# Performance work log

Hardware: AMD Instinct MI355X
Metric: run time of the kernel (lower is better)

Reference implementation:

```python
import jax, jax.numpy as jnp
import numpy as np

N = 10000       # nodes
E = 160000      # edges (avg degree 16)
F_IN = 5        # node feature dim
ED = 2          # edge feature dim


def _tconv(x, src, dst, ea, Wq, bq, Wk, bk, Wv, bv, We, Ws, bs, heads, C, concat):
    """PyG TransformerConv (eval mode, root_weight=True, beta=False)."""
    n = x.shape[0]
    q = (x @ Wq + bq).reshape(n, heads, C)
    k = (x @ Wk + bk).reshape(n, heads, C)
    v = (x @ Wv + bv).reshape(n, heads, C)
    e = (ea @ We).reshape(ea.shape[0], heads, C)          # edge embedding, added to key and value
    kj = k[src] + e                                        # [E,H,C] gather source keys
    vj = v[src] + e                                        # [E,H,C] gather source values
    logits = jnp.einsum('ehc,ehc->eh', q[dst], kj) / jnp.sqrt(jnp.asarray(C, x.dtype))
    m = jax.ops.segment_max(logits, dst, num_segments=n)   # stable segment softmax over in-edges
    p = jnp.exp(logits - m[dst])
    s = jax.ops.segment_sum(p, dst, num_segments=n)
    alpha = p / s[dst]                                     # [E,H]
    out = jax.ops.segment_sum(alpha[..., None] * vj, dst, num_segments=n)  # [N,H,C]
    out = out.reshape(n, heads * C) if concat else jnp.mean(out, axis=1)
    return out + x @ Ws + bs                               # root/skip connection


def setup_inputs() -> dict:
    key = jax.random.key(0)
    keys = iter(jax.random.split(key, 64))
    def p(shape):
        return jax.random.normal(next(keys), shape, jnp.float32) * 0.05
    inp = {}
    inp['x'] = jax.random.normal(next(keys), (N, F_IN), jnp.float32)
    inp['edge_src'] = jax.random.randint(next(keys), (E,), 0, N)
    inp['edge_dst'] = jax.random.randint(next(keys), (E,), 0, N)
    inp['edge_attr'] = jax.random.normal(next(keys), (E, ED), jnp.float32)
    # (in_dim, heads, out_channels, concat) for the 3 TransformerConv layers
    layers = [(F_IN, 4, 128, True), (512, 4, 128, True), (512, 1, 64, False)]
    for i, (fin, h, c, concat) in enumerate(layers, 1):
        hc = h * c
        sk = hc if concat else c
        inp[f'Wq{i}'] = p((fin, hc)); inp[f'bq{i}'] = p((hc,))
        inp[f'Wk{i}'] = p((fin, hc)); inp[f'bk{i}'] = p((hc,))
        inp[f'Wv{i}'] = p((fin, hc)); inp[f'bv{i}'] = p((hc,))
        inp[f'We{i}'] = p((ED, hc))   # lin_edge has no bias in PyG
        inp[f'Ws{i}'] = p((fin, sk)); inp[f'bs{i}'] = p((sk,))
    return inp


def reference(x, edge_src, edge_dst, edge_attr,
              Wq1, bq1, Wk1, bk1, Wv1, bv1, We1, Ws1, bs1,
              Wq2, bq2, Wk2, bk2, Wv2, bv2, We2, Ws2, bs2,
              Wq3, bq3, Wk3, bk3, Wv3, bv3, We3, Ws3, bs3):
    h = jax.nn.relu(_tconv(x, edge_src, edge_dst, edge_attr,
                           Wq1, bq1, Wk1, bk1, Wv1, bv1, We1, Ws1, bs1, 4, 128, True))
    h = jax.nn.relu(_tconv(h, edge_src, edge_dst, edge_attr,
                           Wq2, bq2, Wk2, bk2, Wv2, bv2, We2, Ws2, bs2, 4, 128, True))
    return _tconv(h, edge_src, edge_dst, edge_attr,
                  Wq3, bq3, Wk3, bk3, Wv3, bv3, We3, Ws3, bs3, 1, 64, False)
```

## Files before the change

### kernel.cpp

```cpp
#include <hip/hip_runtime.h>

typedef unsigned short u16;
typedef __attribute__((ext_vector_type(8))) short bf16x8;
typedef __attribute__((ext_vector_type(4))) float f32x4;

__device__ __forceinline__ float bf2f(u16 s) {
    return __uint_as_float(((unsigned)s) << 16);
}
__device__ __forceinline__ u16 f2bf(float f) {
    unsigned u = __float_as_uint(f);
    u += 0x7fff + ((u >> 16) & 1);
    return (u16)(u >> 16);
}
__device__ __forceinline__ void unpack8(bf16x8 x, float* f) {
#pragma unroll
    for (int j = 0; j < 8; ++j) f[j] = bf2f((u16)x[j]);
}

struct Ptr4 { const float* p[4]; };
struct Ptr8 { const float* p[8]; };

__global__ __launch_bounds__(256)
void transpose_cvt4(Ptr4 srcs, u16* __restrict__ dst, int K, int Nw) {
    const float* in = srcs.p[blockIdx.z];
    u16* out = dst + (size_t)blockIdx.z * Nw * K;
    __shared__ float t[32][33];
    int kb = blockIdx.x * 32, nb = blockIdx.y * 32;
    int tx = threadIdx.x & 31, ty = threadIdx.x >> 5;
#pragma unroll
    for (int r = ty; r < 32; r += 8)
        if (kb + r < K && nb + tx < Nw)
            t[r][tx] = in[(size_t)(kb + r) * Nw + nb + tx];
    __syncthreads();
#pragma unroll
    for (int r = ty; r < 32; r += 8)
        if (nb + r < Nw && kb + tx < K)
            out[(size_t)(nb + r) * K + kb + tx] = f2bf(t[tx][r]);
}

__global__ __launch_bounds__(256)
void bias_pack(Ptr8 a, float* __restrict__ b2, float* __restrict__ b3) {
    int j = blockIdx.x * 256 + threadIdx.x;
    if (j < 2048) b2[j] = a.p[j >> 9][j & 511];
    else if (j < 2304) { int jj = j - 2048; b3[jj] = a.p[4 + (jj >> 6)][jj & 63]; }
}

__global__ __launch_bounds__(256)
void gemm_l1(const float* __restrict__ X, Ptr8 wb, u16* __restrict__ OUT, int N) {
    int n = blockIdx.x;
    int wsel = threadIdx.x >> 6;
    int jj = (threadIdx.x & 63) * 8;
    const float* W = wb.p[wsel];
    const float* b = wb.p[4 + wsel];
    float xr[5];
#pragma unroll
    for (int i = 0; i < 5; ++i) xr[i] = X[(size_t)n * 5 + i];
    float acc[8];
#pragma unroll
    for (int j = 0; j < 8; ++j) acc[j] = b[jj + j];
#pragma unroll
    for (int i = 0; i < 5; ++i)
#pragma unroll
        for (int j = 0; j < 8; ++j)
            acc[j] = fmaf(xr[i], W[(size_t)i * 512 + jj + j], acc[j]);
    bf16x8 o;
#pragma unroll
    for (int j = 0; j < 8; ++j) o[j] = (short)f2bf(acc[j]);
    *(bf16x8*)(OUT + (size_t)n * 2048 + wsel * 512 + jj) = o;
}

template <int TN>
__global__ __launch_bounds__(256)
void gemm_bf16(const u16* __restrict__ A, const u16* __restrict__ Bt,
               const float* __restrict__ bias, u16* __restrict__ C,
               int M, int Ncols, int K) {
    constexpr int TM = 128, BK = 64;
    constexpr int MFR = (TN == 128) ? 4 : 2;
    constexpr int NFR = 4;
    constexpr int ACH = TM * BK / (256 * 8);
    constexpr int BCH = TN * BK / (256 * 8);

    __shared__ u16 As[TM * BK];
    __shared__ u16 Bs[TN * BK];

    int tid = threadIdx.x;
    int lane = tid & 63;
    int w = tid >> 6;
    int rowbase = blockIdx.x * TM;
    int colbase = blockIdx.y * TN;
    int mwave = (TN == 128) ? (w >> 1) * 64 : w * 32;
    int nwave = (TN == 128) ? (w & 1) * 64 : 0;

    f32x4 acc[MFR][NFR] = {};

    for (int k0 = 0; k0 < K; k0 += BK) {
        bf16x8 ra[ACH], rb[BCH];
#pragma unroll
        for (int c = 0; c < ACH; ++c) {
            int idx = c * 256 + tid;
            int row = idx >> 3, sl = idx & 7;
            int gr = rowbase + row; if (gr > M - 1) gr = M - 1;
            ra[c] = *(const bf16x8*)(A + (size_t)gr * K + k0 + sl * 8);
        }
#pragma unroll
        for (int c = 0; c < BCH; ++c) {
            int idx = c * 256 + tid;
            int row = idx >> 3, sl = idx & 7;
            rb[c] = *(const bf16x8*)(Bt + (size_t)(colbase + row) * K + k0 + sl * 8);
        }
        __syncthreads();
#pragma unroll
        for (int c = 0; c < ACH; ++c) {
            int idx = c * 256 + tid;
            int row = idx >> 3, sl = idx & 7;
            *(bf16x8*)&As[row * BK + ((sl ^ (row & 7)) * 8)] = ra[c];
        }
#pragma unroll
        for (int c = 0; c < BCH; ++c) {
            int idx = c * 256 + tid;
            int row = idx >> 3, sl = idx & 7;
            *(bf16x8*)&Bs[row * BK + ((sl ^ (row & 7)) * 8)] = rb[c];
        }
        __syncthreads();
#pragma unroll
        for (int kh = 0; kh < 2; ++kh) {
            bf16x8 af[MFR], bfr[NFR];
            int ks = (lane >> 4) + kh * 4;
#pragma unroll
            for (int mi = 0; mi < MFR; ++mi) {
                int r = mwave + mi * 16 + (lane & 15);
                af[mi] = *(const bf16x8*)&As[r * BK + ((ks ^ (r & 7)) * 8)];
            }
#pragma unroll
            for (int ni = 0; ni < NFR; ++ni) {
                int r = nwave + ni * 16 + (lane & 15);
                bfr[ni] = *(const bf16x8*)&Bs[r * BK + ((ks ^ (r & 7)) * 8)];
            }
#pragma unroll
            for (int mi = 0; mi < MFR; ++mi)
#pragma unroll
                for (int ni = 0; ni < NFR; ++ni)
                    acc[mi][ni] = __builtin_amdgcn_mfma_f32_16x16x32_bf16(
                        af[mi], bfr[ni], acc[mi][ni], 0, 0, 0);
        }
    }
#pragma unroll
    for (int mi = 0; mi < MFR; ++mi) {
        int r0 = rowbase + mwave + mi * 16 + (lane >> 4) * 4;
#pragma unroll
        for (int ni = 0; ni < NFR; ++ni) {
            int col = colbase + nwave + ni * 16 + (lane & 15);
            float bv = bias[col];
#pragma unroll
            for (int r = 0; r < 4; ++r) {
                int row = r0 + r;
                if (row < M)
                    C[(size_t)row * Ncols + col] = f2bf(acc[mi][ni][r] + bv);
            }
        }
    }
}

__global__ __launch_bounds__(256)
void histo_dst(const int* __restrict__ dst, int* __restrict__ deg, int E) {
    int i = blockIdx.x * 256 + threadIdx.x;
    if (i < E) atomicAdd(&deg[dst[i]], 1);
}

__global__ __launch_bounds__(1024)
void scan_deg(const int* __restrict__ deg, int* __restrict__ off,
              int* __restrict__ cur, int N) {
    __shared__ int part[1024];
    int t = threadIdx.x;
    int per = (N + 1023) / 1024;
    int base = t * per;
    int s = 0;
    for (int i = 0; i < per; ++i)
        if (base + i < N) s += deg[base + i];
    part[t] = s;
    __syncthreads();
    for (int d = 1; d < 1024; d <<= 1) {
        int v = (t >= d) ? part[t - d] : 0;
        __syncthreads();
        part[t] += v;
        __syncthreads();
    }
    int excl = (t > 0) ? part[t - 1] : 0;
    for (int i = 0; i < per; ++i) {
        int n = base + i;
        if (n < N) {
            off[n] = excl;
            cur[n] = excl;
            excl += deg[n];
        }
    }
    if (t == 1023) off[N] = part[1023];
}

__global__ __launch_bounds__(256)
void scatter_edges(const int* __restrict__ dst, int* __restrict__ cur,
                   int* __restrict__ eid, int E) {
    int i = blockIdx.x * 256 + threadIdx.x;
    if (i < E) {
        int p = atomicAdd(&cur[dst[i]], 1);
        eid[p] = i;
    }
}

template <int H, int C, int LPG, int EPAR, bool RELU, typename OutT>
__global__ __launch_bounds__(256)
void node_attn(const u16* __restrict__ QKVS, int SR, int koff, int voff,
               int skoff, const int* __restrict__ esrc,
               const float* __restrict__ EA, const float* __restrict__ We,
               const int* __restrict__ off, const int* __restrict__ eid,
               OutT* __restrict__ OUT, int OST, int N, float scale) {
    constexpr int HC = H * C;
    constexpr int NG = 64 / LPG;
    int n = blockIdx.x * 4 + (threadIdx.x >> 6);
    if (n >= N) return;
    int lane = threadIdx.x & 63;
    int g = lane / LPG;
    int li = lane % LPG;
    int cc = (EPAR > 1 ? 0 : g) * C + li * 8;

    const u16* nrow = QKVS + (size_t)n * SR;
    float q[8];
    unpack8(*(const bf16x8*)(nrow + cc), q);

    float qw0 = 0.f, qw1 = 0.f;
    {
        f32x4 wa = *(const f32x4*)(We + cc), wb = *(const f32x4*)(We + cc + 4);
        f32x4 wc = *(const f32x4*)(We + HC + cc), wd = *(const f32x4*)(We + HC + cc + 4);
#pragma unroll
        for (int j = 0; j < 4; ++j) {
            qw0 = fmaf(q[j], wa[j], qw0); qw0 = fmaf(q[4 + j], wb[j], qw0);
            qw1 = fmaf(q[j], wc[j], qw1); qw1 = fmaf(q[4 + j], wd[j], qw1);
        }
    }
#pragma unroll
    for (int d = 1; d < LPG; d <<= 1) {
        qw0 += __shfl_xor(qw0, d);
        qw1 += __shfl_xor(qw1, d);
    }

    int base = off[n];
    int deg = off[n + 1] - base;
    int pdeg = deg < 64 ? deg : 64;
    int ps = 0; float pax = 0.f, pay = 0.f;
    if (lane < pdeg) {
        int e = eid[base + lane];
        ps = esrc[e];
        float2 a = *(const float2*)(EA + 2 * (size_t)e);
        pax = a.x; pay = a.y;
    }

    float m = -1e30f, s = 0.f, A0 = 0.f, A1 = 0.f;
    float acc[8] = {};
    const u16* Kp = QKVS + koff;
    const u16* Vp = QKVS + voff;

    auto process = [&](float ax, float ay, bf16x8 k8, bf16x8 v8) {
        float kf[8];
        unpack8(k8, kf);
        float qk = 0.f;
#pragma unroll
        for (int j = 0; j < 8; ++j) qk = fmaf(q[j], kf[j], qk);
#pragma unroll
        for (int d = 1; d < LPG; d <<= 1) qk += __shfl_xor(qk, d);
        float lg = scale * (qk + ax * qw0 + ay * qw1);
        if (lg > m + 8.f) {
            float r = __expf(m - lg);
            s *= r; A0 *= r; A1 *= r;
#pragma unroll
            for (int j = 0; j < 8; ++j) acc[j] *= r;
            m = lg;
        }
        float p = __expf(lg - m);
        s += p;
        A0 = fmaf(p, ax, A0);
        A1 = fmaf(p, ay, A1);
        float vf[8];
        unpack8(v8, vf);
#pragma unroll
        for (int j = 0; j < 8; ++j) acc[j] = fmaf(p, vf[j], acc[j]);
    };

    if constexpr (EPAR == 1) {
        int t = 0;
        for (; t + 1 < pdeg; t += 2) {
            int s0 = __shfl(ps, t), s1 = __shfl(ps, t + 1);
            float ax0 = __shfl(pax, t), ay0 = __shfl(pay, t);
            float ax1 = __shfl(pax, t + 1), ay1 = __shfl(pay, t + 1);
            bf16x8 k0 = *(const bf16x8*)(Kp + (size_t)s0 * SR + cc);
            bf16x8 v0 = *(const bf16x8*)(Vp + (size_t)s0 * SR + cc);
            bf16x8 k1 = *(const bf16x8*)(Kp + (size_t)s1 * SR + cc);
            bf16x8 v1 = *(const bf16x8*)(Vp + (size_t)s1 * SR + cc);
            process(ax0, ay0, k0, v0);
            process(ax1, ay1, k1, v1);
        }
        if (t < pdeg) {
            int s0 = __shfl(ps, t);
            float ax0 = __shfl(pax, t), ay0 = __shfl(pay, t);
            bf16x8 k0 = *(const bf16x8*)(Kp + (size_t)s0 * SR + cc);
            bf16x8 v0 = *(const bf16x8*)(Vp + (size_t)s0 * SR + cc);
            process(ax0, ay0, k0, v0);
        }
        for (t = 64; t < deg; ++t) {
            int e = eid[base + t];
            int s0 = esrc[e];
            float2 a = *(const float2*)(EA + 2 * (size_t)e);
            bf16x8 k0 = *(const bf16x8*)(Kp + (size_t)s0 * SR + cc);
            bf16x8 v0 = *(const bf16x8*)(Vp + (size_t)s0 * SR + cc);
            process(a.x, a.y, k0, v0);
        }
    } else {
        int trips = (pdeg + NG - 1) / NG;
        for (int k = 0; k < trips; ++k) {
            int idx = g + NG * k;
            bool valid = idx < pdeg;
            int sidx = valid ? idx : (pdeg - 1);
            int s0 = __shfl(ps, sidx);
            float ax0 = __shfl(pax, sidx), ay0 = __shfl(pay, sidx);
            bf16x8 k0 = *(const bf16x8*)(Kp + (size_t)s0 * SR + cc);
            bf16x8 v0 = *(const bf16x8*)(Vp + (size_t)s0 * SR + cc);
            if (valid) process(ax0, ay0, k0, v0);
        }
        int otr = (deg > 64) ? (deg - 64 + NG - 1) / NG : 0;
        for (int k = 0; k < otr; ++k) {
            int idx = 64 + NG * k + g;
            bool valid = idx < deg;
            int ii = valid ? idx : (deg - 1);
            int e = eid[base + ii];
            int s0 = esrc[e];
            float2 a = *(const float2*)(EA + 2 * (size_t)e);
            bf16x8 k0 = *(const bf16x8*)(Kp + (size_t)s0 * SR + cc);
            bf16x8 v0 = *(const bf16x8*)(Vp + (size_t)s0 * SR + cc);
            if (valid) process(a.x, a.y, k0, v0);
        }
#pragma unroll
        for (int d = LPG; d < 64; d <<= 1) {
            float mo = __shfl_xor(m, d), so = __shfl_xor(s, d);
            float A0o = __shfl_xor(A0, d), A1o = __shfl_xor(A1, d);
            float mn = fmaxf(m, mo);
            float ra = __expf(m - mn), rb = __expf(mo - mn);
            s = s * ra + so * rb;
            A0 = A0 * ra + A0o * rb;
            A1 = A1 * ra + A1o * rb;
#pragma unroll
            for (int j = 0; j < 8; ++j) {
                float ao = __shfl_xor(acc[j], d);
                acc[j] = acc[j] * ra + ao * rb;
            }
            m = mn;
        }
    }

    if (EPAR == 1 || g == 0) {
        float inv = (s > 0.f) ? 1.f / s : 0.f;
        float sk[8];
        unpack8(*(const bf16x8*)(nrow + skoff + cc), sk);
        f32x4 wa = *(const f32x4*)(We + cc), wb = *(const f32x4*)(We + cc + 4);
        f32x4 wc = *(const f32x4*)(We + HC + cc), wd = *(const f32x4*)(We + HC + cc + 4);
        float w0[8] = {wa[0], wa[1], wa[2], wa[3], wb[0], wb[1], wb[2], wb[3]};
        float w1[8] = {wc[0], wc[1], wc[2], wc[3], wd[0], wd[1], wd[2], wd[3]};
        float o[8];
#pragma unroll
        for (int j = 0; j < 8; ++j) {
            float agg = (acc[j] + A0 * w0[j] + A1 * w1[j]) * inv;
            o[j] = agg + sk[j];
            if (RELU) o[j] = fmaxf(o[j], 0.f);
        }
        if constexpr (sizeof(OutT) == 2) {
            bf16x8 ov;
#pragma unroll
            for (int j = 0; j < 8; ++j) ov[j] = (short)f2bf(o[j]);
            *(bf16x8*)((u16*)OUT + (size_t)n * OST + cc) = ov;
        } else {
            f32x4 oa = {o[0], o[1], o[2], o[3]}, ob = {o[4], o[5], o[6], o[7]};
            *(f32x4*)((float*)OUT + (size_t)n * OST + cc) = oa;
            *(f32x4*)((float*)OUT + (size_t)n * OST + cc + 4) = ob;
        }
    }
}

extern "C" void kernel_launch(void* const* d_in, const int* in_sizes, int n_in,
                              void* d_out, int out_size, void* d_ws, size_t ws_size,
                              hipStream_t stream) {
    const float* x  = (const float*)d_in[0];
    const int* esrc = (const int*)d_in[1];
    const int* edst = (const int*)d_in[2];
    const float* ea = (const float*)d_in[3];
    const int N = in_sizes[0] / 5;
    const int E = in_sizes[1];
    auto in = [&](int i) { return (const float*)d_in[i]; };

    char* p = (char*)d_ws;
    auto alloc = [&](size_t b) {
        char* r = p; p += (b + 255) & ~(size_t)255; return (void*)r;
    };
    u16* QKVS = (u16*)alloc((size_t)N * 2048 * 2);
    u16* HB   = (u16*)alloc((size_t)N * 512 * 2);
    u16* Wt2  = (u16*)alloc((size_t)2048 * 512 * 2);
    u16* Wt3  = (u16*)alloc((size_t)256 * 512 * 2);
    float* b2 = (float*)alloc(2048 * 4);
    float* b3 = (float*)alloc(256 * 4);
    int* deg  = (int*)alloc((size_t)N * 4);
    int* off  = (int*)alloc((size_t)(N + 1) * 4);
    int* cur  = (int*)alloc((size_t)N * 4);
    int* eid  = (int*)alloc((size_t)E * 4);

    dim3 b256(256);
    int gE256 = (E + 255) / 256;
    int gM = (N + 127) / 128;
    int gA = (N + 3) / 4;
    const float scale128 = 0.08838834764831845f;
    const float scale64  = 0.125f;

    hipMemsetAsync(deg, 0, (size_t)N * sizeof(int), stream);
    histo_dst<<<gE256, b256, 0, stream>>>(edst, deg, E);
    scan_deg<<<1, 1024, 0, stream>>>(deg, off, cur, N);
    scatter_edges<<<gE256, b256, 0, stream>>>(edst, cur, eid, E);

    Ptr4 w2 = {{in(13), in(15), in(17), in(20)}};
    Ptr4 w3 = {{in(22), in(24), in(26), in(29)}};
    Ptr8 bb = {{in(14), in(16), in(18), in(21), in(23), in(25), in(27), in(30)}};
    transpose_cvt4<<<dim3(16, 16, 4), b256, 0, stream>>>(w2, Wt2, 512, 512);
    transpose_cvt4<<<dim3(16, 2, 4),  b256, 0, stream>>>(w3, Wt3, 512, 64);
    bias_pack<<<dim3(9), b256, 0, stream>>>(bb, b2, b3);

    Ptr8 l1 = {{in(4), in(6), in(8), in(11), in(5), in(7), in(9), in(12)}};
    gemm_l1<<<dim3(N), b256, 0, stream>>>(x, l1, QKVS, N);
    node_attn<4, 128, 16, 1, true, u16><<<dim3(gA), b256, 0, stream>>>(
        QKVS, 2048, 512, 1024, 1536, esrc, ea, in(10), off, eid, HB, 512, N, scale128);

    gemm_bf16<128><<<dim3(gM, 16), b256, 0, stream>>>(HB, Wt2, b2, QKVS, N, 2048, 512);
    node_attn<4, 128, 16, 1, true, u16><<<dim3(gA), b256, 0, stream>>>(
        QKVS, 2048, 512, 1024, 1536, esrc, ea, in(19), off, eid, HB, 512, N, scale128);

    gemm_bf16<64><<<dim3(gM, 4), b256, 0, stream>>>(HB, Wt3, b3, QKVS, N, 256, 512);
    node_attn<1, 64, 8, 8, false, float><<<dim3(gA), b256, 0, stream>>>(
        QKVS, 256, 64, 128, 192, esrc, ea, in(28), off, eid,
        (float*)d_out, 64, N, scale64);
}
```

Baseline: 246.7 us.

## Pre-gather edge src/attrs into CSR order, prefetch K/V, merge prep kernels

The edge scatter now writes source indices and edge attributes directly in CSR order, so the attention kernels read them contiguously instead of chasing eid->esrc/EA. The EPAR=1 attention loop is software-pipelined, keeping four edges' K/V loads in flight ahead of use. The weight transpose and bias pack kernels are merged into one launch, and the layer-1 GEMM processes 8 nodes per block with weights held in registers. In exchange the scatter writes more data, and the prefetch adds register pressure plus redundant loads of edge 0 when an index runs past the degree.

```diff
diff --git a/kernel.cpp b/kernel.cpp
--- a/kernel.cpp
+++ b/kernel.cpp
@@ -17,56 +17,74 @@
     for (int j = 0; j < 8; ++j) f[j] = bf2f((u16)x[j]);
 }
 
-struct Ptr4 { const float* p[4]; };
 struct Ptr8 { const float* p[8]; };
-
-__global__ __launch_bounds__(256)
-void transpose_cvt4(Ptr4 srcs, u16* __restrict__ dst, int K, int Nw) {
-    const float* in = srcs.p[blockIdx.z];
-    u16* out = dst + (size_t)blockIdx.z * Nw * K;
+struct PrepArgs { const float* w[8]; const float* b[8]; };
+
+__global__ __launch_bounds__(256)
+void prep_weights(PrepArgs a, u16* __restrict__ Wt2, u16* __restrict__ Wt3,
+                  float* __restrict__ b2, float* __restrict__ b3) {
+    int z = blockIdx.z;
+    if (z == 8) {
+        if (blockIdx.y != 0 || blockIdx.x >= 9) return;
+        int j = blockIdx.x * 256 + threadIdx.x;
+        if (j < 2048) b2[j] = a.b[j >> 9][j & 511];
+        else if (j < 2304) { int jj = j - 2048; b3[jj] = a.b[4 + (jj >> 6)][jj & 63]; }
+        return;
+    }
+    const float* in;
+    u16* out;
+    int Nw;
+    if (z < 4) { in = a.w[z]; out = Wt2 + (size_t)z * 512 * 512; Nw = 512; }
+    else {
+        if (blockIdx.y >= 2) return;
+        in = a.w[z]; out = Wt3 + (size_t)(z - 4) * 64 * 512; Nw = 64;
+    }
     __shared__ float t[32][33];
     int kb = blockIdx.x * 32, nb = blockIdx.y * 32;
     int tx = threadIdx.x & 31, ty = threadIdx.x >> 5;
 #pragma unroll
     for (int r = ty; r < 32; r += 8)
-        if (kb + r < K && nb + tx < Nw)
+        if (nb + tx < Nw)
             t[r][tx] = in[(size_t)(kb + r) * Nw + nb + tx];
     __syncthreads();
 #pragma unroll
     for (int r = ty; r < 32; r += 8)
-        if (nb + r < Nw && kb + tx < K)
-            out[(size_t)(nb + r) * K + kb + tx] = f2bf(t[tx][r]);
-}
-
-__global__ __launch_bounds__(256)
-void bias_pack(Ptr8 a, float* __restrict__ b2, float* __restrict__ b3) {
-    int j = blockIdx.x * 256 + threadIdx.x;
-    if (j < 2048) b2[j] = a.p[j >> 9][j & 511];
-    else if (j < 2304) { int jj = j - 2048; b3[jj] = a.p[4 + (jj >> 6)][jj & 63]; }
+        if (nb + r < Nw)
+            out[(size_t)(nb + r) * 512 + kb + tx] = f2bf(t[tx][r]);
 }
 
 __global__ __launch_bounds__(256)
 void gemm_l1(const float* __restrict__ X, Ptr8 wb, u16* __restrict__ OUT, int N) {
-    int n = blockIdx.x;
     int wsel = threadIdx.x >> 6;
     int jj = (threadIdx.x & 63) * 8;
     const float* W = wb.p[wsel];
     const float* b = wb.p[4 + wsel];
-    float xr[5];
-#pragma unroll
-    for (int i = 0; i < 5; ++i) xr[i] = X[(size_t)n * 5 + i];
-    float acc[8];
-#pragma unroll
-    for (int j = 0; j < 8; ++j) acc[j] = b[jj + j];
+    float w[5][8], bs[8];
 #pragma unroll
     for (int i = 0; i < 5; ++i)
 #pragma unroll
-        for (int j = 0; j < 8; ++j)
-            acc[j] = fmaf(xr[i], W[(size_t)i * 512 + jj + j], acc[j]);
-    bf16x8 o;
-#pragma unroll
-    for (int j = 0; j < 8; ++j) o[j] = (short)f2bf(acc[j]);
-    *(bf16x8*)(OUT + (size_t)n * 2048 + wsel * 512 + jj) = o;
+        for (int j = 0; j < 8; ++j) w[i][j] = W[(size_t)i * 512 + jj + j];
+#pragma unroll
+    for (int j = 0; j < 8; ++j) bs[j] = b[jj + j];
+    int n0 = blockIdx.x * 8;
+    int nend = (N - n0 < 8) ? (N - n0) : 8;
+    for (int i = 0; i < nend; ++i) {
+        int n = n0 + i;
+        float xr[5];
+#pragma unroll
+        for (int k = 0; k < 5; ++k) xr[k] = X[(size_t)n * 5 + k];
+        float acc[8];
+#pragma unroll
+        for (int j = 0; j < 8; ++j) acc[j] = bs[j];
+#pragma unroll
+        for (int k = 0; k < 5; ++k)
+#pragma unroll
+            for (int j = 0; j < 8; ++j) acc[j] = fmaf(xr[k], w[k][j], acc[j]);
+        bf16x8 o;
+#pragma unroll
+        for (int j = 0; j < 8; ++j) o[j] = (short)f2bf(acc[j]);
+        *(bf16x8*)(OUT + (size_t)n * 2048 + wsel * 512 + jj) = o;
+    }
 }
 
 template <int TN>
@@ -198,22 +216,24 @@
 }
 
 __global__ __launch_bounds__(256)
-void scatter_edges(const int* __restrict__ dst, int* __restrict__ cur,
-                   int* __restrict__ eid, int E) {
+void scatter_edges(const int* __restrict__ src, const int* __restrict__ dst,
+                   const float* __restrict__ EA, int* __restrict__ cur,
+                   int* __restrict__ csrc, float2* __restrict__ caxy, int E) {
     int i = blockIdx.x * 256 + threadIdx.x;
     if (i < E) {
         int p = atomicAdd(&cur[dst[i]], 1);
-        eid[p] = i;
+        csrc[p] = src[i];
+        caxy[p] = *(const float2*)(EA + 2 * (size_t)i);
     }
 }
 
 template <int H, int C, int LPG, int EPAR, bool RELU, typename OutT>
 __global__ __launch_bounds__(256)
 void node_attn(const u16* __restrict__ QKVS, int SR, int koff, int voff,
-               int skoff, const int* __restrict__ esrc,
-               const float* __restrict__ EA, const float* __restrict__ We,
-               const int* __restrict__ off, const int* __restrict__ eid,
-               OutT* __restrict__ OUT, int OST, int N, float scale) {
+               int skoff, const int* __restrict__ csrc,
+               const float2* __restrict__ caxy, const float* __restrict__ We,
+               const int* __restrict__ off, OutT* __restrict__ OUT,
+               int OST, int N, float scale) {
     constexpr int HC = H * C;
     constexpr int NG = 64 / LPG;
     int n = blockIdx.x * 4 + (threadIdx.x >> 6);
@@ -248,9 +268,8 @@
     int pdeg = deg < 64 ? deg : 64;
     int ps = 0; float pax = 0.f, pay = 0.f;
     if (lane < pdeg) {
-        int e = eid[base + lane];
-        ps = esrc[e];
-        float2 a = *(const float2*)(EA + 2 * (size_t)e);
+        ps = csrc[base + lane];
+        float2 a = caxy[base + lane];
         pax = a.x; pay = a.y;
     }
 
@@ -286,29 +305,44 @@
     };
 
     if constexpr (EPAR == 1) {
-        int t = 0;
-        for (; t + 1 < pdeg; t += 2) {
-            int s0 = __shfl(ps, t), s1 = __shfl(ps, t + 1);
-            float ax0 = __shfl(pax, t), ay0 = __shfl(pay, t);
-            float ax1 = __shfl(pax, t + 1), ay1 = __shfl(pay, t + 1);
-            bf16x8 k0 = *(const bf16x8*)(Kp + (size_t)s0 * SR + cc);
-            bf16x8 v0 = *(const bf16x8*)(Vp + (size_t)s0 * SR + cc);
-            bf16x8 k1 = *(const bf16x8*)(Kp + (size_t)s1 * SR + cc);
-            bf16x8 v1 = *(const bf16x8*)(Vp + (size_t)s1 * SR + cc);
-            process(ax0, ay0, k0, v0);
-            process(ax1, ay1, k1, v1);
-        }
-        if (t < pdeg) {
-            int s0 = __shfl(ps, t);
-            float ax0 = __shfl(pax, t), ay0 = __shfl(pay, t);
-            bf16x8 k0 = *(const bf16x8*)(Kp + (size_t)s0 * SR + cc);
-            bf16x8 v0 = *(const bf16x8*)(Vp + (size_t)s0 * SR + cc);
-            process(ax0, ay0, k0, v0);
-        }
-        for (t = 64; t < deg; ++t) {
-            int e = eid[base + t];
-            int s0 = esrc[e];
-            float2 a = *(const float2*)(EA + 2 * (size_t)e);
+        auto ldp = [&](int t, bf16x8& k8, bf16x8& v8) {
+            int tt = t < pdeg ? t : 0;
+            int s0 = __shfl(ps, tt);
+            k8 = *(const bf16x8*)(Kp + (size_t)s0 * SR + cc);
+            v8 = *(const bf16x8*)(Vp + (size_t)s0 * SR + cc);
+        };
+        if (pdeg > 0) {
+            bf16x8 ka0, va0, ka1, va1, kb0, vb0, kb1, vb1;
+            ldp(0, ka0, va0); ldp(1, ka1, va1);
+            ldp(2, kb0, vb0); ldp(3, kb1, vb1);
+            int t = 0;
+            for (; t + 2 < pdeg; t += 4) {
+                float ax, ay;
+                ax = __shfl(pax, t); ay = __shfl(pay, t);
+                process(ax, ay, ka0, va0);
+                ax = __shfl(pax, t + 1); ay = __shfl(pay, t + 1);
+                process(ax, ay, ka1, va1);
+                ldp(t + 4, ka0, va0); ldp(t + 5, ka1, va1);
+                ax = __shfl(pax, t + 2); ay = __shfl(pay, t + 2);
+                process(ax, ay, kb0, vb0);
+                if (t + 3 < pdeg) {
+                    ax = __shfl(pax, t + 3); ay = __shfl(pay, t + 3);
+                    process(ax, ay, kb1, vb1);
+                }
+                ldp(t + 6, kb0, vb0); ldp(t + 7, kb1, vb1);
+            }
+            if (t < pdeg) {
+                float ax = __shfl(pax, t), ay = __shfl(pay, t);
+                process(ax, ay, ka0, va0);
+            }
+            if (t + 1 < pdeg) {
+                float ax = __shfl(pax, t + 1), ay = __shfl(pay, t + 1);
+                process(ax, ay, ka1, va1);
+            }
+        }
+        for (int t = 64; t < deg; ++t) {
+            int s0 = csrc[base + t];
+            float2 a = caxy[base + t];
             bf16x8 k0 = *(const bf16x8*)(Kp + (size_t)s0 * SR + cc);
             bf16x8 v0 = *(const bf16x8*)(Vp + (size_t)s0 * SR + cc);
             process(a.x, a.y, k0, v0);
@@ -330,9 +364,8 @@
             int idx = 64 + NG * k + g;
             bool valid = idx < deg;
             int ii = valid ? idx : (deg - 1);
-            int e = eid[base + ii];
-            int s0 = esrc[e];
-            float2 a = *(const float2*)(EA + 2 * (size_t)e);
+            int s0 = csrc[base + ii];
+            float2 a = caxy[base + ii];
             bf16x8 k0 = *(const bf16x8*)(Kp + (size_t)s0 * SR + cc);
             bf16x8 v0 = *(const bf16x8*)(Vp + (size_t)s0 * SR + cc);
             if (valid) process(a.x, a.y, k0, v0);
@@ -398,16 +431,17 @@
     auto alloc = [&](size_t b) {
         char* r = p; p += (b + 255) & ~(size_t)255; return (void*)r;
     };
-    u16* QKVS = (u16*)alloc((size_t)N * 2048 * 2);
-    u16* HB   = (u16*)alloc((size_t)N * 512 * 2);
-    u16* Wt2  = (u16*)alloc((size_t)2048 * 512 * 2);
-    u16* Wt3  = (u16*)alloc((size_t)256 * 512 * 2);
-    float* b2 = (float*)alloc(2048 * 4);
-    float* b3 = (float*)alloc(256 * 4);
-    int* deg  = (int*)alloc((size_t)N * 4);
-    int* off  = (int*)alloc((size_t)(N + 1) * 4);
-    int* cur  = (int*)alloc((size_t)N * 4);
-    int* eid  = (int*)alloc((size_t)E * 4);
+    u16* QKVS  = (u16*)alloc((size_t)N * 2048 * 2);
+    u16* HB    = (u16*)alloc((size_t)N * 512 * 2);
+    u16* Wt2   = (u16*)alloc((size_t)2048 * 512 * 2);
+    u16* Wt3   = (u16*)alloc((size_t)256 * 512 * 2);
+    float* b2  = (float*)alloc(2048 * 4);
+    float* b3  = (float*)alloc(256 * 4);
+    int* deg   = (int*)alloc((size_t)N * 4);
+    int* off   = (int*)alloc((size_t)(N + 1) * 4);
+    int* cur   = (int*)alloc((size_t)N * 4);
+    int* csrc  = (int*)alloc((size_t)E * 4);
+    float2* caxy = (float2*)alloc((size_t)E * 8);
 
     dim3 b256(256);
     int gE256 = (E + 255) / 256;
@@ -419,26 +453,23 @@
     hipMemsetAsync(deg, 0, (size_t)N * sizeof(int), stream);
     histo_dst<<<gE256, b256, 0, stream>>>(edst, deg, E);
     scan_deg<<<1, 1024, 0, stream>>>(deg, off, cur, N);
-    scatter_edges<<<gE256, b256, 0, stream>>>(edst, cur, eid, E);
-
-    Ptr4 w2 = {{in(13), in(15), in(17), in(20)}};
-    Ptr4 w3 = {{in(22), in(24), in(26), in(29)}};
-    Ptr8 bb = {{in(14), in(16), in(18), in(21), in(23), in(25), in(27), in(30)}};
-    transpose_cvt4<<<dim3(16, 16, 4), b256, 0, stream>>>(w2, Wt2, 512, 512);
-    transpose_cvt4<<<dim3(16, 2, 4),  b256, 0, stream>>>(w3, Wt3, 512, 64);
-    bias_pack<<<dim3(9), b256, 0, stream>>>(bb, b2, b3);
+    scatter_edges<<<gE256, b256, 0, stream>>>(esrc, edst, ea, cur, csrc, caxy, E);
+
+    PrepArgs pa = {{in(13), in(15), in(17), in(20), in(22), in(24), in(26), in(29)},
+                   {in(14), in(16), in(18), in(21), in(23), in(25), in(27), in(30)}};
+    prep_weights<<<dim3(16, 16, 9), b256, 0, stream>>>(pa, Wt2, Wt3, b2, b3);
 
     Ptr8 l1 = {{in(4), in(6), in(8), in(11), in(5), in(7), in(9), in(12)}};
-    gemm_l1<<<dim3(N), b256, 0, stream>>>(x, l1, QKVS, N);
+    gemm_l1<<<dim3((N + 7) / 8), b256, 0, stream>>>(x, l1, QKVS, N);
     node_attn<4, 128, 16, 1, true, u16><<<dim3(gA), b256, 0, stream>>>(
-        QKVS, 2048, 512, 1024, 1536, esrc, ea, in(10), off, eid, HB, 512, N, scale128);
+        QKVS, 2048, 512, 1024, 1536, csrc, caxy, in(10), off, HB, 512, N, scale128);
 
     gemm_bf16<128><<<dim3(gM, 16), b256, 0, stream>>>(HB, Wt2, b2, QKVS, N, 2048, 512);
     node_attn<4, 128, 16, 1, true, u16><<<dim3(gA), b256, 0, stream>>>(
-        QKVS, 2048, 512, 1024, 1536, esrc, ea, in(19), off, eid, HB, 512, N, scale128);
+        QKVS, 2048, 512, 1024, 1536, csrc, caxy, in(19), off, HB, 512, N, scale128);
 
     gemm_bf16<64><<<dim3(gM, 4), b256, 0, stream>>>(HB, Wt3, b3, QKVS, N, 256, 512);
     node_attn<1, 64, 8, 8, false, float><<<dim3(gA), b256, 0, stream>>>(
-        QKVS, 256, 64, 128, 192, esrc, ea, in(28), off, eid,
+        QKVS, 256, 64, 128, 192, csrc, caxy, in(28), off,
         (float*)d_out, 64, N, scale64);
 }
```

Result: faster. 225.8 us (-8.4%).
